# Kernel tuning notes

Measured on AMD Instinct MI355X. Metric: run time of the kernel, lower is better.

Reference implementation:

```python
import jax, jax.numpy as jnp
import numpy as np
import math

B, S, D, H, L, DFF = 32, 512, 1024, 16, 4, 4096
DK = D // H  # 64


def setup_inputs() -> dict:
    key = jax.random.key(0)
    ks = jax.random.split(key, 8)
    sc = 0.02
    w = lambda k, shp: (jax.random.normal(k, shp, jnp.float32) * sc)
    return dict(
        q_embed_data=jax.random.normal(ks[0], (B, S, D), jnp.float32),
        qa_embed_data=jax.random.normal(ks[1], (B, S, D), jnp.float32),
        Wk=w(ks[2], (L, D, D)), bk=jnp.zeros((L, D), jnp.float32),
        Wv=w(ks[3], (L, D, D)), bv=jnp.zeros((L, D), jnp.float32),
        Wo=w(ks[4], (L, D, D)), bo=jnp.zeros((L, D), jnp.float32),
        g1=jnp.ones((L, D), jnp.float32), be1=jnp.zeros((L, D), jnp.float32),
        W1=w(ks[5], (L, D, DFF)), c1=jnp.zeros((L, DFF), jnp.float32),
        W2=w(ks[6], (L, DFF, D)), c2=jnp.zeros((L, D), jnp.float32),
        g2=jnp.ones((L, D), jnp.float32), be2=jnp.zeros((L, D), jnp.float32),
    )


def _posemb(seqlen, d_model):
    # sinusoidal table (the 0.1*randn init is fully overwritten since d_model is even)
    pos = jnp.arange(seqlen, dtype=jnp.float32)[:, None]
    div = jnp.exp(jnp.arange(0, d_model, 2, dtype=jnp.float32) * (-math.log(10000.0) / d_model))
    pe = jnp.zeros((seqlen, d_model), jnp.float32)
    pe = pe.at[:, 0::2].set(jnp.sin(pos * div)).at[:, 1::2].set(jnp.cos(pos * div))
    return pe


def _ln(x, g, b, eps=1e-5):
    m = jnp.mean(x, axis=-1, keepdims=True)
    v = jnp.mean(jnp.square(x - m), axis=-1, keepdims=True)
    return (x - m) * jax.lax.rsqrt(v + eps) * g + b


def reference(q_embed_data, qa_embed_data, Wk, bk, Wv, bv, Wo, bo,
              g1, be1, W1, c1, W2, c2, g2, be2):
    pe = _posemb(S, D)
    x = q_embed_data + pe          # query/key stream
    y = qa_embed_data + pe         # value stream (constant across blocks)
    idx = jnp.arange(S)
    allowed = idx[:, None] > idx[None, :]  # strictly-past: triu(k=0) masked incl. diagonal

    def block(x, p):
        Wk_, bk_, Wv_, bv_, Wo_, bo_, g1_, be1_, W1_, c1_, W2_, c2_, g2_, be2_ = p
        # kq_same=1: q and k both use k_linear
        qh = (x @ Wk_ + bk_).reshape(B, S, H, DK).transpose(0, 2, 1, 3)
        kh = qh
        vh = (y @ Wv_ + bv_).reshape(B, S, H, DK).transpose(0, 2, 1, 3)
        scores = jnp.einsum('bhid,bhjd->bhij', qh, kh) / math.sqrt(DK)
        attn = jax.nn.softmax(jnp.where(allowed, scores, -1e32), axis=-1)
        # zero_pad trick: row 0 of attention is replaced by zeros
        attn = attn.at[:, :, 0, :].set(0.0)
        out = jnp.einsum('bhij,bhjd->bhid', attn, vh)
        out = out.transpose(0, 2, 1, 3).reshape(B, S, D) @ Wo_ + bo_
        x = _ln(x + out, g1_, be1_)
        ffn = jax.nn.relu(x @ W1_ + c1_) @ W2_ + c2_
        x = _ln(x + ffn, g2_, be2_)
        return x, None

    x, _ = jax.lax.scan(block, x, (Wk, bk, Wv, bv, Wo, bo, g1, be1, W1, c1, W2, c2, g2, be2))
    return x
```

## Files before the change

### kernel.cpp

```cpp
#include <hip/hip_runtime.h>


#define DEV static __device__ __forceinline__

typedef unsigned short u16;
typedef __attribute__((ext_vector_type(4))) unsigned short u16x4;
typedef __attribute__((ext_vector_type(8))) unsigned short u16x8;
typedef __attribute__((ext_vector_type(8))) short bf16x8;
typedef __attribute__((ext_vector_type(4))) float f32x4;

static constexpr int Bn = 32, Sn = 512, Dn = 1024, Hn = 16, Ln = 4, DFFn = 4096, DKn = 64;
static constexpr int Mn = Bn * Sn;

DEV u16 f2bf(float f) {
  unsigned u = __float_as_uint(f);
  u += 0x7FFFu + ((u >> 16) & 1u);
  return (u16)(u >> 16);
}
DEV float bf2f(u16 v) { return __uint_as_float((unsigned)v << 16); }

DEV void gload_lds16(const void* g, void* l) {
  __builtin_amdgcn_global_load_lds((const __attribute__((address_space(1))) void*)g,
                                   (__attribute__((address_space(3))) void*)l, 16, 0, 0);
}

DEV void barf() {
  asm volatile("" ::: "memory");
  __builtin_amdgcn_s_barrier();
  asm volatile("" ::: "memory");
}

__global__ __launch_bounds__(256) void pe_add_kernel(
    const float* __restrict__ q, const float* __restrict__ qa,
    float* __restrict__ x, u16* __restrict__ xb, u16* __restrict__ yb)
{
  size_t i4 = ((size_t)blockIdx.x * 256 + threadIdx.x) * 4;
  int d0 = (int)(i4 & (Dn - 1));
  int s  = (int)((i4 >> 10) & (Sn - 1));
  float p = (float)s;
  const float LC = 0.0089944730195f;
  float a0 = p * expf(-LC * (float)d0);
  float a2 = p * expf(-LC * (float)(d0 + 2));
  float pe0 = sinf(a0), pe1 = cosf(a0), pe2 = sinf(a2), pe3 = cosf(a2);
  const float4 qv = *(const float4*)(q + i4);
  const float4 av = *(const float4*)(qa + i4);
  float x0 = qv.x + pe0, x1 = qv.y + pe1, x2 = qv.z + pe2, x3 = qv.w + pe3;
  float y0 = av.x + pe0, y1 = av.y + pe1, y2 = av.z + pe2, y3 = av.w + pe3;
  *(float4*)(x + i4) = make_float4(x0, x1, x2, x3);
  u16x4 xv4 = { f2bf(x0), f2bf(x1), f2bf(x2), f2bf(x3) };
  u16x4 yv4 = { f2bf(y0), f2bf(y1), f2bf(y2), f2bf(y3) };
  *(u16x4*)(xb + i4) = xv4;
  *(u16x4*)(yb + i4) = yv4;
}

__global__ __launch_bounds__(256) void transpose_cast_kernel(
    const float* __restrict__ in, u16* __restrict__ out, int R, int C)
{
  __shared__ float t[32][33];
  int tx = threadIdx.x & 31, ty = threadIdx.x >> 5;
  int c0 = blockIdx.x * 32, r0 = blockIdx.y * 32;
  #pragma unroll
  for (int i = 0; i < 4; ++i)
    t[ty + i * 8][tx] = in[(size_t)(r0 + ty + i * 8) * C + c0 + tx];
  __syncthreads();
  #pragma unroll
  for (int i = 0; i < 4; ++i) {
    int rr = ty + i * 8;
    out[(size_t)(c0 + rr) * R + r0 + tx] = f2bf(t[tx][rr]);
  }
}

__global__ __launch_bounds__(256) void transpose_cast3_kernel(
    const float* __restrict__ i0, const float* __restrict__ i1, const float* __restrict__ i2,
    u16* __restrict__ o0, u16* __restrict__ o1, u16* __restrict__ o2)
{
  const int z = blockIdx.z;
  const float* in = (z == 0) ? i0 : (z == 1) ? i1 : i2;
  u16* out = (z == 0) ? o0 : (z == 1) ? o1 : o2;
  __shared__ float t[32][33];
  int tx = threadIdx.x & 31, ty = threadIdx.x >> 5;
  int c0 = blockIdx.x * 32, r0 = blockIdx.y * 32;
  #pragma unroll
  for (int i = 0; i < 4; ++i)
    t[ty + i * 8][tx] = in[(size_t)(r0 + ty + i * 8) * Dn + c0 + tx];
  __syncthreads();
  #pragma unroll
  for (int i = 0; i < 4; ++i) {
    int rr = ty + i * 8;
    out[(size_t)(c0 + rr) * Dn + r0 + tx] = f2bf(t[tx][rr]);
  }
}

template<int BIAS, int RELU, int F32OUT, int ACC, int DUAL = 0, int VTR = 0>
__global__ __launch_bounds__(512, 2) void gemm8p_kernel(
    const u16* __restrict__ A, int lda,
    const u16* __restrict__ BT, int ldb,
    const float* __restrict__ bias,
    void* __restrict__ Cout, int ldc,
    int M, int N, int K,
    const u16* A2 = nullptr, const u16* BT2 = nullptr,
    const float* bias2 = nullptr, void* Cout2 = nullptr)
{
  if (DUAL && blockIdx.z) { A = A2; BT = BT2; bias = bias2; Cout = Cout2; }
  const bool vtr = VTR && DUAL && blockIdx.z;
  __shared__ u16 lds[2][2][16384];
  const int tid = threadIdx.x;
  const int lane = tid & 63, wid = tid >> 6;
  const int g = lane >> 4, r16 = lane & 15;
  const int wm = wid >> 2, wn = wid & 3;

  const int nwgx = N >> 8;
  const int nwg = gridDim.x * gridDim.y;
  const int flat = blockIdx.y * gridDim.x + blockIdx.x;
  const int cpx = nwg >> 3;
  const int logical = (flat & 7) * cpx + (flat >> 3);
  const int n0 = (logical % nwgx) << 8;
  const int m0 = (logical / nwgx) << 8;

  f32x4 acc[8][4];
  #pragma unroll
  for (int i = 0; i < 8; ++i)
    #pragma unroll
    for (int j = 0; j < 4; ++j) acc[i][j] = (f32x4){0.f, 0.f, 0.f, 0.f};

  const int rr = tid >> 3, ck = tid & 7;
  const int scol = ((ck ^ (rr & 7)) << 3);
  const u16* Asrc = A  + (size_t)(m0 + rr) * lda + scol;
  const u16* Bsrc = BT + (size_t)(n0 + rr) * ldb + scol;
  const int eds = rr * 64 + ck * 8;
  const size_t a64 = (size_t)64 * lda, b64 = (size_t)64 * ldb;

  #define STG(p, h, t) do {                                                  \
    if ((h) < 2) {                                                           \
      const u16* s_ = Asrc + (size_t)((h) * 128) * lda + (t) * 64;           \
      gload_lds16(s_,       &lds[p][0][eds + (h) * 8192]);                   \
      gload_lds16(s_ + a64, &lds[p][0][eds + (h) * 8192 + 4096]);            \
    } else {                                                                 \
      const u16* s_ = Bsrc + (size_t)(((h) - 2) * 128) * ldb + (t) * 64;     \
      gload_lds16(s_,       &lds[p][1][eds + ((h) - 2) * 8192]);             \
      gload_lds16(s_ + b64, &lds[p][1][eds + ((h) - 2) * 8192 + 4096]);      \
    }                                                                        \
  } while (0)

  const int c0 = ((g ^ (r16 & 7)) << 3);
  const int c1 = (((4 + g) ^ (r16 & 7)) << 3);
  const int arow = wm * 128 + r16;
  const int brow = wn * 64 + r16;

  #define LDA2(p, q, af) do {                                                        \
    af[0][0] = *(const bf16x8*)&lds[p][0][(arow + (2*(q))   * 16) * 64 + c0];        \
    af[0][1] = *(const bf16x8*)&lds[p][0][(arow + (2*(q))   * 16) * 64 + c1];        \
    af[1][0] = *(const bf16x8*)&lds[p][0][(arow + (2*(q)+1) * 16) * 64 + c0];        \
    af[1][1] = *(const bf16x8*)&lds[p][0][(arow + (2*(q)+1) * 16) * 64 + c1];        \
  } while (0)

  #define MMQ(q, af, bf) do {                                                        \
    __builtin_amdgcn_s_setprio(1);                                                   \
    _Pragma("unroll")                                                                \
    for (int ks = 0; ks < 2; ++ks)                                                   \
      _Pragma("unroll")                                                              \
      for (int i2 = 0; i2 < 2; ++i2)                                                 \
        _Pragma("unroll")                                                            \
        for (int j = 0; j < 4; ++j)                                                  \
          acc[2*(q)+i2][j] = __builtin_amdgcn_mfma_f32_16x16x32_bf16(af[i2][ks], bf[j][ks], acc[2*(q)+i2][j], 0, 0, 0); \
    __builtin_amdgcn_s_setprio(0);                                                   \
  } while (0)

  const int nt = K >> 6;
  STG(0, 0, 0); STG(0, 1, 0); STG(0, 2, 0); STG(0, 3, 0);
  asm volatile("s_waitcnt vmcnt(0)" ::: "memory");
  barf();

  for (int t = 0; t < nt; ++t) {
    const int p = t & 1;
    const bool pf = (t + 1 < nt);
    bf16x8 bf[4][2], af[2][2], ag[2][2];
    #pragma unroll
    for (int j = 0; j < 4; ++j) {
      bf[j][0] = *(const bf16x8*)&lds[p][1][(brow + j * 16) * 64 + c0];
      bf[j][1] = *(const bf16x8*)&lds[p][1][(brow + j * 16) * 64 + c1];
    }
    LDA2(p, 0, af);
    if (pf) { STG(p ^ 1, 0, t + 1); STG(p ^ 1, 1, t + 1); }
    MMQ(0, af, bf);
    LDA2(p, 1, ag);
    if (pf) STG(p ^ 1, 2, t + 1);
    MMQ(1, ag, bf);
    LDA2(p, 2, af);
    if (pf) STG(p ^ 1, 3, t + 1);
    MMQ(2, af, bf);
    LDA2(p, 3, ag);
    MMQ(3, ag, bf);
    asm volatile("s_waitcnt lgkmcnt(0)" ::: "memory");
    asm volatile("s_waitcnt vmcnt(0)" ::: "memory");
    barf();
  }
  #undef STG
  #undef LDA2
  #undef MMQ

  #pragma unroll
  for (int i = 0; i < 8; ++i) {
    const int rb = m0 + wm * 128 + i * 16 + 4 * g;
    #pragma unroll
    for (int j = 0; j < 4; ++j) {
      const int col = n0 + wn * 64 + j * 16 + r16;
      float badd = BIAS ? bias[col] : 0.f;
      if (vtr) {
        u16x4 pk;
        #pragma unroll
        for (int r = 0; r < 4; ++r) pk[r] = f2bf(acc[i][j][r] + badd);
        const int h_ = col >> 6, dk = col & 63;
        const int b_ = rb >> 9, s0 = rb & (Sn - 1);
        *(u16x4*)&((u16*)Cout)[(((size_t)(b_ * Hn + h_) * DKn + dk) << 9) + s0] = pk;
      } else {
        #pragma unroll
        for (int r = 0; r < 4; ++r) {
          size_t off = (size_t)(rb + r) * ldc + col;
          float v = acc[i][j][r] + badd;
          if (RELU) v = fmaxf(v, 0.f);
          if (F32OUT) {
            float* Cf = (float*)Cout;
            if (ACC) v += Cf[off];
            Cf[off] = v;
          } else {
            ((u16*)Cout)[off] = f2bf(v);
          }
        }
      }
    }
  }
}

__global__ __launch_bounds__(512) void fattn_kernel(
    const u16* __restrict__ Kb, const u16* __restrict__ Vt, u16* __restrict__ O)
{
  __shared__ u16 kl[64][72];
  __shared__ u16 vl[64][72];
  __shared__ u16 pw[8][16][72];
  const int idx = blockIdx.x;
  const int qt = idx & 3;
  const int h  = (idx >> 2) & 15;
  const int b  = idx >> 6;
  const int Q0 = qt * 128;
  const int tid = threadIdx.x;
  const int lane = tid & 63, w = tid >> 6;
  const int g = lane >> 4, r16 = lane & 15;
  const int myrow = Q0 + 16 * w;

  bf16x8 qf[2];
  {
    const u16* qrow = &Kb[(size_t)(b * Sn + myrow + r16) * Dn + h * DKn];
    qf[0] = *(const bf16x8*)(qrow + 8 * g);
    qf[1] = *(const bf16x8*)(qrow + 32 + 8 * g);
  }
  f32x4 oacc[4];
  float mrow[4], lrow[4];
  #pragma unroll
  for (int j = 0; j < 4; ++j) oacc[j] = (f32x4){0.f, 0.f, 0.f, 0.f};
  #pragma unroll
  for (int r = 0; r < 4; ++r) { mrow[r] = -1e30f; lrow[r] = 0.f; }

  const int srow = tid >> 3;
  const int scol = (tid & 7) * 8;
  const u16* kbase = Kb + (size_t)(b * Sn) * Dn + h * DKn;
  const u16* vbase = Vt + (size_t)(b * Hn + h) * DKn * Sn;
  const int ctmax = 2 * qt + 1;

  for (int ct = 0; ct <= ctmax; ++ct) {
    __syncthreads();
    *(u16x8*)&kl[srow][scol] = *(const u16x8*)&kbase[(size_t)(ct * 64 + srow) * Dn + scol];
    *(u16x8*)&vl[srow][scol] = *(const u16x8*)&vbase[(size_t)srow * Sn + ct * 64 + scol];
    __syncthreads();
    if (ct * 64 > myrow + 14) continue;

    f32x4 sa[4];
    #pragma unroll
    for (int j = 0; j < 4; ++j) {
      sa[j] = (f32x4){0.f, 0.f, 0.f, 0.f};
      #pragma unroll
      for (int ks = 0; ks < 2; ++ks) {
        bf16x8 kf = *(const bf16x8*)&kl[16 * j + r16][32 * ks + 8 * g];
        sa[j] = __builtin_amdgcn_mfma_f32_16x16x32_bf16(qf[ks], kf, sa[j], 0, 0, 0);
      }
    }
    const bool needmask = (ct * 64 + 63 >= myrow);
    float p4[4][4];
    #pragma unroll
    for (int j = 0; j < 4; ++j)
      #pragma unroll
      for (int r = 0; r < 4; ++r) {
        float v = sa[j][r] * 0.125f;
        if (needmask && (ct * 64 + 16 * j + r16 >= myrow + 4 * g + r)) v = -3e38f;
        p4[j][r] = v;
      }
    #pragma unroll
    for (int r = 0; r < 4; ++r) {
      float m = fmaxf(fmaxf(p4[0][r], p4[1][r]), fmaxf(p4[2][r], p4[3][r]));
      #pragma unroll
      for (int o = 8; o; o >>= 1) m = fmaxf(m, __shfl_xor(m, o));
      float mn = fmaxf(mrow[r], m);
      float sc = __expf(mrow[r] - mn);
      mrow[r] = mn;
      float s = 0.f;
      #pragma unroll
      for (int j = 0; j < 4; ++j) {
        float e = __expf(p4[j][r] - mn);
        p4[j][r] = e;
        s += e;
      }
      #pragma unroll
      for (int o = 8; o; o >>= 1) s += __shfl_xor(s, o);
      lrow[r] = lrow[r] * sc + s;
      #pragma unroll
      for (int j = 0; j < 4; ++j) oacc[j][r] *= sc;
    }
    #pragma unroll
    for (int j = 0; j < 4; ++j)
      #pragma unroll
      for (int r = 0; r < 4; ++r)
        pw[w][4 * g + r][16 * j + r16] = f2bf(p4[j][r]);
    #pragma unroll
    for (int ks = 0; ks < 2; ++ks) {
      bf16x8 pa = *(const bf16x8*)&pw[w][r16][32 * ks + 8 * g];
      #pragma unroll
      for (int j = 0; j < 4; ++j) {
        bf16x8 vb = *(const bf16x8*)&vl[16 * j + r16][32 * ks + 8 * g];
        oacc[j] = __builtin_amdgcn_mfma_f32_16x16x32_bf16(pa, vb, oacc[j], 0, 0, 0);
      }
    }
  }
  #pragma unroll
  for (int r = 0; r < 4; ++r) {
    float inv = (lrow[r] > 0.f) ? 1.f / lrow[r] : 0.f;
    #pragma unroll
    for (int j = 0; j < 4; ++j)
      O[(size_t)(b * Sn + myrow + 4 * g + r) * Dn + h * DKn + 16 * j + r16] =
          f2bf(oacc[j][r] * inv);
  }
}

template<int TBF>
__global__ __launch_bounds__(256) void ln_kernel(
    const float* __restrict__ xin, const void* __restrict__ tin,
    const float* __restrict__ pb, const float* __restrict__ gam,
    const float* __restrict__ bet, float* __restrict__ xout, u16* __restrict__ xbout)
{
  const int row = blockIdx.x;
  const int tid = threadIdx.x;
  const size_t base = (size_t)row * Dn + tid * 4;
  float4 xv = *(const float4*)(xin + base);
  float4 tv;
  if (TBF) {
    u16x4 t4 = *(const u16x4*)((const u16*)tin + base);
    tv = make_float4(bf2f(t4[0]), bf2f(t4[1]), bf2f(t4[2]), bf2f(t4[3]));
  } else {
    tv = *(const float4*)((const float*)tin + base);
  }
  float4 bb = *(const float4*)(pb + tid * 4);
  float v0 = xv.x + tv.x + bb.x, v1 = xv.y + tv.y + bb.y;
  float v2 = xv.z + tv.z + bb.z, v3 = xv.w + tv.w + bb.w;
  float s  = v0 + v1 + v2 + v3;
  float s2 = v0 * v0 + v1 * v1 + v2 * v2 + v3 * v3;
  #pragma unroll
  for (int o = 32; o > 0; o >>= 1) { s += __shfl_xor(s, o); s2 += __shfl_xor(s2, o); }
  __shared__ float rs[4], rs2[4];
  const int wid = tid >> 6;
  if ((tid & 63) == 0) { rs[wid] = s; rs2[wid] = s2; }
  __syncthreads();
  s  = rs[0] + rs[1] + rs[2] + rs[3];
  s2 = rs2[0] + rs2[1] + rs2[2] + rs2[3];
  const float mean = s * (1.f / Dn);
  const float var  = s2 * (1.f / Dn) - mean * mean;
  const float rstd = rsqrtf(fmaxf(var, 0.f) + 1e-5f);
  float4 gv = *(const float4*)(gam + tid * 4);
  float4 bv = *(const float4*)(bet + tid * 4);
  float o0 = (v0 - mean) * rstd * gv.x + bv.x;
  float o1 = (v1 - mean) * rstd * gv.y + bv.y;
  float o2 = (v2 - mean) * rstd * gv.z + bv.z;
  float o3 = (v3 - mean) * rstd * gv.w + bv.w;
  *(float4*)(xout + base) = make_float4(o0, o1, o2, o3);
  u16x4 ub = { f2bf(o0), f2bf(o1), f2bf(o2), f2bf(o3) };
  *(u16x4*)(xbout + base) = ub;
}

extern "C" void kernel_launch(void* const* d_in, const int* in_sizes, int n_in,
                              void* d_out, int out_size, void* d_ws, size_t ws_size,
                              hipStream_t stream)
{
  const float* q   = (const float*)d_in[0];
  const float* qa  = (const float*)d_in[1];
  const float* Wk  = (const float*)d_in[2];
  const float* bk  = (const float*)d_in[3];
  const float* Wv  = (const float*)d_in[4];
  const float* bv  = (const float*)d_in[5];
  const float* Wo  = (const float*)d_in[6];
  const float* bo  = (const float*)d_in[7];
  const float* g1  = (const float*)d_in[8];
  const float* be1 = (const float*)d_in[9];
  const float* W1  = (const float*)d_in[10];
  const float* c1  = (const float*)d_in[11];
  const float* W2  = (const float*)d_in[12];
  const float* c2  = (const float*)d_in[13];
  const float* g2  = (const float*)d_in[14];
  const float* be2 = (const float*)d_in[15];
  float* x = (float*)d_out;

  const size_t MD  = (size_t)Mn * Dn;
  const size_t MF  = (size_t)Mn * DFFn;
  const size_t WSZ = 3 * (size_t)Dn * Dn * 2 + 2 * (size_t)Dn * DFFn * 2;
  const size_t NEED_SMALL = 5 * MD * 2 + WSZ + 8192;
  const size_t NEED_BIG   = 2 * MD * 2 + MF * 2 + MD * 4 + WSZ + 8192;
  if (ws_size < NEED_SMALL) return;
  const bool big = (ws_size >= NEED_BIG);

  char* wsb = (char*)d_ws;
  size_t off = 0;
  auto take = [&](size_t bytes) -> void* {
    void* r = wsb + off;
    off += (bytes + 255) & ~(size_t)255;
    return r;
  };
  u16 *XB, *YB, *KB, *VT, *VB, *H1 = nullptr;
  float* TMP;
  XB = (u16*)take(MD * 2);
  YB = (u16*)take(MD * 2);
  if (big) {
    H1  = (u16*)take(MF * 2);
    TMP = (float*)take(MD * 4);
    KB  = H1;
    VT  = H1 + MD;
    VB  = H1 + 2 * MD;
  } else {
    KB  = (u16*)take(MD * 2);
    VT  = (u16*)take(MD * 2);
    VB  = (u16*)take(MD * 2);
    TMP = (float*)KB;
  }
  u16* WKT = (u16*)take((size_t)Dn * Dn * 2);
  u16* WVT = (u16*)take((size_t)Dn * Dn * 2);
  u16* WOT = (u16*)take((size_t)Dn * Dn * 2);
  u16* W1T = (u16*)take((size_t)Dn * DFFn * 2);
  u16* W2T = (u16*)take((size_t)Dn * DFFn * 2);
  u16* H1C = VB;
  u16* TMPB = (u16*)TMP;
  (void)in_sizes; (void)n_in; (void)out_size;

  pe_add_kernel<<<Mn * Dn / 1024, 256, 0, stream>>>(q, qa, x, XB, YB);

  const dim3 g256(Dn / 256, Mn / 256);
  const dim3 g256z(Dn / 256, Mn / 256, 2);
  const dim3 gW1(DFFn / 256, Mn / 256);
  for (int l = 0; l < Ln; ++l) {
    const size_t wo = (size_t)l * Dn * Dn;
    const size_t fo = (size_t)l * Dn * DFFn;
    transpose_cast3_kernel<<<dim3(32, 32, 3), 256, 0, stream>>>(
        Wk + wo, Wv + wo, Wo + wo, WKT, WVT, WOT);
    transpose_cast_kernel<<<dim3(128, 32), 256, 0, stream>>>(W1 + fo, W1T, Dn, DFFn);
    transpose_cast_kernel<<<dim3(32, 128), 256, 0, stream>>>(W2 + fo, W2T, DFFn, Dn);

    gemm8p_kernel<1,0,0,0,1,1><<<g256z, 512, 0, stream>>>(
        XB, Dn, WKT, Dn, bk + l * Dn, KB, Dn, Mn, Dn, Dn,
        YB, WVT, bv + l * Dn, VT);
    fattn_kernel<<<Bn * Hn * 4, 512, 0, stream>>>(KB, VT, VB);
    if (big) {
      gemm8p_kernel<0,0,0,0><<<g256, 512, 0, stream>>>(VB, Dn, WOT, Dn, nullptr, TMPB, Dn, Mn, Dn, Dn);
      ln_kernel<1><<<Mn, 256, 0, stream>>>(x, TMPB, bo + l * Dn, g1 + l * Dn, be1 + l * Dn, x, XB);
      gemm8p_kernel<1,1,0,0><<<gW1, 512, 0, stream>>>(
          XB, Dn, W1T, Dn, c1 + l * DFFn, H1, DFFn, Mn, DFFn, Dn);
      gemm8p_kernel<0,0,0,0><<<g256, 512, 0, stream>>>(
          H1, DFFn, W2T, DFFn, nullptr, TMPB, Dn, Mn, Dn, DFFn);
      ln_kernel<1><<<Mn, 256, 0, stream>>>(x, TMPB, c2 + l * Dn, g2 + l * Dn, be2 + l * Dn, x, XB);
    } else {
      gemm8p_kernel<0,0,1,0><<<g256, 512, 0, stream>>>(VB, Dn, WOT, Dn, nullptr, TMP, Dn, Mn, Dn, Dn);
      ln_kernel<0><<<Mn, 256, 0, stream>>>(x, TMP, bo + l * Dn, g1 + l * Dn, be1 + l * Dn, x, XB);
      for (int ci = 0; ci < 4; ++ci) {
        gemm8p_kernel<1,1,0,0><<<g256, 512, 0, stream>>>(
            XB, Dn, W1T + (size_t)ci * Dn * Dn, Dn, c1 + l * DFFn + ci * Dn, H1C, Dn, Mn, Dn, Dn);
        if (ci == 0)
          gemm8p_kernel<0,0,1,0><<<g256, 512, 0, stream>>>(
              H1C, Dn, W2T + (size_t)ci * Dn, DFFn, nullptr, TMP, Dn, Mn, Dn, Dn);
        else
          gemm8p_kernel<0,0,1,1><<<g256, 512, 0, stream>>>(
              H1C, Dn, W2T + (size_t)ci * Dn, DFFn, nullptr, TMP, Dn, Mn, Dn, Dn);
      }
      ln_kernel<0><<<Mn, 256, 0, stream>>>(x, TMP, c2 + l * Dn, g2 + l * Dn, be2 + l * Dn, x, XB);
    }
  }
}
```

Baseline: 2.186 ms.

## Prefetch next K/V tile into registers and defer softmax rescaling in attention

The attention loop now issues global loads for the next K/V tile into registers before computing on the current LDS tile, then writes them to LDS after a barrier, so memory latency overlaps with MFMA and softmax work. It also adds a lazy-rescale rule: the running max is only updated when the new tile max exceeds it by more than 8, which skips the exp and accumulator rescale in most iterations. s_setprio hints are placed around the MFMA sections. This costs extra registers that may reduce occupancy, and the deferred max lets unnormalized values grow by up to e^8 in bf16 P and fp32 accumulators.

```diff
diff --git a/kernel.cpp b/kernel.cpp
--- a/kernel.cpp
+++ b/kernel.cpp
@@ -267,67 +267,92 @@
   const u16* vbase = Vt + (size_t)(b * Hn + h) * DKn * Sn;
   const int ctmax = 2 * qt + 1;
 
+  {
+    u16x8 k0 = *(const u16x8*)&kbase[(size_t)srow * Dn + scol];
+    u16x8 v0 = *(const u16x8*)&vbase[(size_t)srow * Sn + scol];
+    *(u16x8*)&kl[srow][scol] = k0;
+    *(u16x8*)&vl[srow][scol] = v0;
+  }
+  __syncthreads();
+
   for (int ct = 0; ct <= ctmax; ++ct) {
-    __syncthreads();
-    *(u16x8*)&kl[srow][scol] = *(const u16x8*)&kbase[(size_t)(ct * 64 + srow) * Dn + scol];
-    *(u16x8*)&vl[srow][scol] = *(const u16x8*)&vbase[(size_t)srow * Sn + ct * 64 + scol];
-    __syncthreads();
-    if (ct * 64 > myrow + 14) continue;
-
-    f32x4 sa[4];
-    #pragma unroll
-    for (int j = 0; j < 4; ++j) {
-      sa[j] = (f32x4){0.f, 0.f, 0.f, 0.f};
+    u16x8 kn, vn;
+    const bool pf = (ct + 1 <= ctmax);
+    if (pf) {
+      kn = *(const u16x8*)&kbase[(size_t)((ct + 1) * 64 + srow) * Dn + scol];
+      vn = *(const u16x8*)&vbase[(size_t)srow * Sn + (ct + 1) * 64 + scol];
+    }
+    if (ct * 64 <= myrow + 14) {
+      f32x4 sa[4];
+      __builtin_amdgcn_s_setprio(1);
+      #pragma unroll
+      for (int j = 0; j < 4; ++j) {
+        sa[j] = (f32x4){0.f, 0.f, 0.f, 0.f};
+        #pragma unroll
+        for (int ks = 0; ks < 2; ++ks) {
+          bf16x8 kf = *(const bf16x8*)&kl[16 * j + r16][32 * ks + 8 * g];
+          sa[j] = __builtin_amdgcn_mfma_f32_16x16x32_bf16(qf[ks], kf, sa[j], 0, 0, 0);
+        }
+      }
+      __builtin_amdgcn_s_setprio(0);
+      const bool needmask = (ct * 64 + 63 >= myrow);
+      float p4[4][4];
+      #pragma unroll
+      for (int j = 0; j < 4; ++j)
+        #pragma unroll
+        for (int r = 0; r < 4; ++r) {
+          float v = sa[j][r] * 0.125f;
+          if (needmask && (ct * 64 + 16 * j + r16 >= myrow + 4 * g + r)) v = -3e38f;
+          p4[j][r] = v;
+        }
+      #pragma unroll
+      for (int r = 0; r < 4; ++r) {
+        float m = fmaxf(fmaxf(p4[0][r], p4[1][r]), fmaxf(p4[2][r], p4[3][r]));
+        #pragma unroll
+        for (int o = 8; o; o >>= 1) m = fmaxf(m, __shfl_xor(m, o));
+        const bool defer = (m <= mrow[r] + 8.f);
+        const float mn = defer ? mrow[r] : m;
+        float s = 0.f;
+        #pragma unroll
+        for (int j = 0; j < 4; ++j) {
+          float e = __expf(p4[j][r] - mn);
+          p4[j][r] = e;
+          s += e;
+        }
+        #pragma unroll
+        for (int o = 8; o; o >>= 1) s += __shfl_xor(s, o);
+        if (defer) {
+          lrow[r] += s;
+        } else {
+          const float sc = __expf(mrow[r] - mn);
+          mrow[r] = mn;
+          lrow[r] = lrow[r] * sc + s;
+          #pragma unroll
+          for (int j = 0; j < 4; ++j) oacc[j][r] *= sc;
+        }
+      }
+      #pragma unroll
+      for (int j = 0; j < 4; ++j)
+        #pragma unroll
+        for (int r = 0; r < 4; ++r)
+          pw[w][4 * g + r][16 * j + r16] = f2bf(p4[j][r]);
+      __builtin_amdgcn_s_setprio(1);
       #pragma unroll
       for (int ks = 0; ks < 2; ++ks) {
-        bf16x8 kf = *(const bf16x8*)&kl[16 * j + r16][32 * ks + 8 * g];
-        sa[j] = __builtin_amdgcn_mfma_f32_16x16x32_bf16(qf[ks], kf, sa[j], 0, 0, 0);
+        bf16x8 pa = *(const bf16x8*)&pw[w][r16][32 * ks + 8 * g];
+        #pragma unroll
+        for (int j = 0; j < 4; ++j) {
+          bf16x8 vb = *(const bf16x8*)&vl[16 * j + r16][32 * ks + 8 * g];
+          oacc[j] = __builtin_amdgcn_mfma_f32_16x16x32_bf16(pa, vb, oacc[j], 0, 0, 0);
+        }
       }
+      __builtin_amdgcn_s_setprio(0);
     }
-    const bool needmask = (ct * 64 + 63 >= myrow);
-    float p4[4][4];
-    #pragma unroll
-    for (int j = 0; j < 4; ++j)
-      #pragma unroll
-      for (int r = 0; r < 4; ++r) {
-        float v = sa[j][r] * 0.125f;
-        if (needmask && (ct * 64 + 16 * j + r16 >= myrow + 4 * g + r)) v = -3e38f;
-        p4[j][r] = v;
-      }
-    #pragma unroll
-    for (int r = 0; r < 4; ++r) {
-      float m = fmaxf(fmaxf(p4[0][r], p4[1][r]), fmaxf(p4[2][r], p4[3][r]));
-      #pragma unroll
-      for (int o = 8; o; o >>= 1) m = fmaxf(m, __shfl_xor(m, o));
-      float mn = fmaxf(mrow[r], m);
-      float sc = __expf(mrow[r] - mn);
-      mrow[r] = mn;
-      float s = 0.f;
-      #pragma unroll
-      for (int j = 0; j < 4; ++j) {
-        float e = __expf(p4[j][r] - mn);
-        p4[j][r] = e;
-        s += e;
-      }
-      #pragma unroll
-      for (int o = 8; o; o >>= 1) s += __shfl_xor(s, o);
-      lrow[r] = lrow[r] * sc + s;
-      #pragma unroll
-      for (int j = 0; j < 4; ++j) oacc[j][r] *= sc;
-    }
-    #pragma unroll
-    for (int j = 0; j < 4; ++j)
-      #pragma unroll
-      for (int r = 0; r < 4; ++r)
-        pw[w][4 * g + r][16 * j + r16] = f2bf(p4[j][r]);
-    #pragma unroll
-    for (int ks = 0; ks < 2; ++ks) {
-      bf16x8 pa = *(const bf16x8*)&pw[w][r16][32 * ks + 8 * g];
-      #pragma unroll
-      for (int j = 0; j < 4; ++j) {
-        bf16x8 vb = *(const bf16x8*)&vl[16 * j + r16][32 * ks + 8 * g];
-        oacc[j] = __builtin_amdgcn_mfma_f32_16x16x32_bf16(pa, vb, oacc[j], 0, 0, 0);
-      }
+    __syncthreads();
+    if (pf) {
+      *(u16x8*)&kl[srow][scol] = kn;
+      *(u16x8*)&vl[srow][scol] = vn;
+      __syncthreads();
     }
   }
   #pragma unroll
```

Result: no change. 2.168 ms (-0.8%).
